# Optimization experiments

Measured on AMD Instinct MI355X. Metric: run time of the kernel, lower is better.

The kernel has to match this reference:

```python
import jax, jax.numpy as jnp
import numpy as np

B, S, HID = 1, 2048, 2048
N_HEADS = 16
HEAD_DIM = HID // N_HEADS  # 128
ROPE_THETA = 10000.0
NEG_INF = -1e9


def setup_inputs() -> dict:
    key = jax.random.key(0)
    ks = jax.random.split(key, 5)
    hidden_states = jax.random.normal(ks[0], (B, S, HID), dtype=jnp.float32)
    scale = 1.0 / np.sqrt(HID)
    Wq = jax.random.normal(ks[1], (HID, HID), dtype=jnp.float32) * scale
    Wk = jax.random.normal(ks[2], (HID, HID), dtype=jnp.float32) * scale
    Wv = jax.random.normal(ks[3], (HID, HID), dtype=jnp.float32) * scale
    Wo = jax.random.normal(ks[4], (HID, HID), dtype=jnp.float32) * scale
    # additive causal mask [B, 1, S, S]: 0 on/below diag, -1e9 above
    causal = jnp.tril(jnp.ones((S, S), dtype=bool))
    attention_mask = jnp.where(causal, 0.0, NEG_INF).astype(jnp.float32)[None, None]
    attention_mask = jnp.broadcast_to(attention_mask, (B, 1, S, S))
    position_ids = jnp.broadcast_to(jnp.arange(S, dtype=jnp.int64)[None, :], (B, S))
    return {"hidden_states": hidden_states, "Wq": Wq, "Wk": Wk, "Wv": Wv,
            "Wo": Wo, "attention_mask": attention_mask, "position_ids": position_ids}


def _rotate_half(x):
    x1, x2 = jnp.split(x, 2, axis=-1)
    return jnp.concatenate((-x2, x1), axis=-1)


def _rope_cos_sin(position_ids, head_dim, dtype):
    inv_freq = 1.0 / (ROPE_THETA ** (jnp.arange(0, head_dim, 2, dtype=jnp.float32) / head_dim))
    freqs = position_ids.astype(jnp.float32)[:, :, None] * inv_freq[None, None, :]  # [b, s, d/2]
    emb = jnp.concatenate((freqs, freqs), axis=-1)  # [b, s, d]
    # unsqueeze_dim=1 -> broadcast over heads
    return jnp.cos(emb).astype(dtype)[:, None], jnp.sin(emb).astype(dtype)[:, None]


def reference(hidden_states, Wq, Wk, Wv, Wo, attention_mask, position_ids):
    b, s, h = hidden_states.shape
    d = HEAD_DIM
    def proj(W):
        return (hidden_states @ W.T).reshape(b, s, N_HEADS, d).transpose(0, 2, 1, 3)  # [b,h,s,d]
    q, k, v = proj(Wq), proj(Wk), proj(Wv)
    cos, sin = _rope_cos_sin(position_ids, d, q.dtype)
    q = q * cos + _rotate_half(q) * sin
    k = k * cos + _rotate_half(k) * sin
    scores = jnp.einsum('bhqd,bhkd->bhqk', q, k) / jnp.sqrt(jnp.float32(d))
    scores = scores + attention_mask
    probs = jax.nn.softmax(scores.astype(jnp.float32), axis=-1).astype(q.dtype)
    attn = jnp.einsum('bhqk,bhkd->bhqd', probs, v)
    out = attn.transpose(0, 2, 1, 3).reshape(b, s, h)
    return out @ Wo.T
```

## Files before the change

### kernel.cpp

```cpp
#include <hip/hip_runtime.h>

typedef _Float16 half8 __attribute__((ext_vector_type(8)));
typedef _Float16 half4 __attribute__((ext_vector_type(4)));
typedef float floatx4 __attribute__((ext_vector_type(4)));
typedef float floatx16 __attribute__((ext_vector_type(16)));

#define GLDS(gp, lp) __builtin_amdgcn_global_load_lds( \
    (const __attribute__((address_space(1))) void*)(gp), \
    (__attribute__((address_space(3))) void*)(lp), 16, 0, 0)

__global__ void cvt_f2h5(const float* __restrict__ s0, const float* __restrict__ s1,
                         const float* __restrict__ s2, const float* __restrict__ s3,
                         const float* __restrict__ s4,
                         _Float16* __restrict__ d0, _Float16* __restrict__ d1,
                         _Float16* __restrict__ d2, _Float16* __restrict__ d3,
                         _Float16* __restrict__ d4, int n8) {
  int i = blockIdx.x * 256 + threadIdx.x;
  if (i >= n8) return;
  const float* s; _Float16* d;
  switch (blockIdx.y) {
    case 0: s = s0; d = d0; break;
    case 1: s = s1; d = d1; break;
    case 2: s = s2; d = d2; break;
    case 3: s = s3; d = d3; break;
    default: s = s4; d = d4; break;
  }
  const float4* s4p = (const float4*)s;
  float4 a = s4p[2 * i], b = s4p[2 * i + 1];
  half8 h;
  h[0] = (_Float16)a.x; h[1] = (_Float16)a.y; h[2] = (_Float16)a.z; h[3] = (_Float16)a.w;
  h[4] = (_Float16)b.x; h[5] = (_Float16)b.y; h[6] = (_Float16)b.z; h[7] = (_Float16)b.w;
  *(half8*)(d + 8 * (size_t)i) = h;
}

__global__ __launch_bounds__(256) void rope_tr(_Float16* __restrict__ Q,
                                               _Float16* __restrict__ K,
                                               const _Float16* __restrict__ V,
                                               _Float16* __restrict__ Vt) {
  __shared__ _Float16 t[64][72];
  const int bid = (int)blockIdx.x;
  if (bid < 8192) {
    const int idx = bid * 256 + threadIdx.x;
    const int s = idx >> 10;
    const int hd = idx & 1023;
    const int head = hd >> 6, d = hd & 63;
    const float freq = exp2f((float)d * -0.2076205059304601f);
    const float ang = (float)s * freq;
    float sn, c;
    __sincosf(ang, &sn, &c);
    const size_t base = (size_t)s * 2048 + head * 128 + d;
    float q1 = (float)Q[base], q2 = (float)Q[base + 64];
    Q[base]      = (_Float16)(q1 * c - q2 * sn);
    Q[base + 64] = (_Float16)(q2 * c + q1 * sn);
    float k1 = (float)K[base], k2 = (float)K[base + 64];
    K[base]      = (_Float16)(k1 * c - k2 * sn);
    K[base + 64] = (_Float16)(k2 * c + k1 * sn);
  } else {
    const int b2 = bid - 8192;
    const int r0 = (b2 >> 5) * 64, c0 = (b2 & 31) * 64;
    const int tr = threadIdx.x >> 3, tc = (threadIdx.x & 7) * 8;
    #pragma unroll
    for (int p = 0; p < 2; ++p) {
      half8 v = *(const half8*)(V + (size_t)(r0 + p * 32 + tr) * 2048 + c0 + tc);
      *(half8*)&t[p * 32 + tr][tc] = v;
    }
    __syncthreads();
    #pragma unroll
    for (int p = 0; p < 2; ++p) {
      half8 v;
      #pragma unroll
      for (int j = 0; j < 8; ++j) v[j] = t[tc + j][p * 32 + tr];
      *(half8*)(Vt + (size_t)(c0 + p * 32 + tr) * 2048 + r0 + tc) = v;
    }
  }
}

__global__ __launch_bounds__(512, 1) void gemm_qkv(const _Float16* __restrict__ A,
                                                   const _Float16* __restrict__ W,
                                                   _Float16* __restrict__ Cq) {
  extern __shared__ _Float16 lds[];
  _Float16* As = lds;
  _Float16* Bs = lds + 3 * 16384;

  const int tid = threadIdx.x, lane = tid & 63, wv = tid >> 6;
  const int fr = lane & 15, fg = lane >> 4;
  const int wm = wv >> 1, wn = wv & 1;
  const int bm = blockIdx.y * 256, bn = blockIdx.x * 192;
  const _Float16* Ab = A + (size_t)bm * 2048;
  const _Float16* Bb = W + (size_t)bn * 2048;

  const int srow = lane >> 3;
  const int sgr = (lane & 7) ^ srow;

  auto stageA = [&](int t) {
    _Float16* dst = As + (t % 3) * 16384;
    const size_t coff = (size_t)t * 64 + sgr * 8;
    #pragma unroll
    for (int i = 0; i < 4; ++i) {
      const int rb = wv * 32 + i * 8;
      GLDS(Ab + (size_t)(rb + srow) * 2048 + coff, dst + rb * 64);
    }
  };
  auto stageB = [&](int t) {
    _Float16* dst = Bs + (t & 1) * 12288;
    const size_t coff = (size_t)t * 64 + sgr * 8;
    #pragma unroll
    for (int i = 0; i < 3; ++i) {
      const int rb = wv * 24 + i * 8;
      GLDS(Bb + (size_t)(rb + srow) * 2048 + coff, dst + rb * 64);
    }
  };

  const int arow = wm * 64 + fr;
  const int brow = wn * 96 + fr;
  const int sw = fr & 7;

  floatx4 acc[4][6] = {};

  stageA(0); stageB(0); stageA(1);
  asm volatile("s_waitcnt vmcnt(4)" ::: "memory");
  __builtin_amdgcn_s_barrier();

  for (int t = 0; t < 32; ++t) {
    const _Float16* Ac = As + (t % 3) * 16384;
    const _Float16* Bc = Bs + (t & 1) * 12288;
    half8 af[2][4], bf[2][6];
    #pragma unroll
    for (int kh = 0; kh < 2; ++kh) {
      const int sl = ((kh * 4 + fg) ^ sw) * 8;
      #pragma unroll
      for (int m = 0; m < 4; ++m)
        af[kh][m] = *(const half8*)(Ac + (arow + m * 16) * 64 + sl);
      #pragma unroll
      for (int n = 0; n < 6; ++n)
        bf[kh][n] = *(const half8*)(Bc + (brow + n * 16) * 64 + sl);
    }
    if (t + 1 < 32) stageB(t + 1);
    if (t + 2 < 32) stageA(t + 2);
    __builtin_amdgcn_s_setprio(1);
    #pragma unroll
    for (int kh = 0; kh < 2; ++kh)
      #pragma unroll
      for (int m = 0; m < 4; ++m)
        #pragma unroll
        for (int n = 0; n < 6; ++n)
          acc[m][n] = __builtin_amdgcn_mfma_f32_16x16x32_f16(af[kh][m], bf[kh][n],
                                                             acc[m][n], 0, 0, 0);
    __builtin_amdgcn_s_setprio(0);
    if (t < 30)       asm volatile("s_waitcnt vmcnt(4)" ::: "memory");
    else if (t == 30) asm volatile("s_waitcnt vmcnt(0)" ::: "memory");
    __builtin_amdgcn_s_barrier();
  }

  #pragma unroll
  for (int m = 0; m < 4; ++m)
    #pragma unroll
    for (int n = 0; n < 6; ++n)
      #pragma unroll
      for (int i = 0; i < 4; ++i) {
        const int row = bm + wm * 64 + m * 16 + fg * 4 + i;
        const int col = bn + wn * 96 + n * 16 + fr;
        Cq[(size_t)(col >> 11) * 4194304 + (size_t)row * 2048 + (col & 2047)] =
            (_Float16)acc[m][n][i];
      }
}

__global__ __launch_bounds__(256, 3) void gemm_o(const _Float16* __restrict__ A,
                                                 const _Float16* __restrict__ B,
                                                 float* __restrict__ out) {
  extern __shared__ _Float16 lds[];
  _Float16* As = lds;
  _Float16* Bs = lds + 3 * 4096;

  const int tid = threadIdx.x, lane = tid & 63, wv = tid >> 6;
  const int fr = lane & 15, fg = lane >> 4;
  const int wm = (wv >> 1) * 64, wn = (wv & 1) * 64;
  const int bm = blockIdx.y * 128, bn = blockIdx.x * 128;
  const _Float16* Ab = A + (size_t)bm * 2048;
  const _Float16* Bb = B + (size_t)bn * 2048;

  const int srow = lane >> 2;
  const int gsw = (lane & 3) ^ ((lane >> 3) & 3);
  const int asw = (fr >> 1) & 3;

  auto stageA = [&](int t) {
    _Float16* dst = As + (t % 3) * 4096;
    const size_t coff = (size_t)t * 32 + gsw * 8;
    #pragma unroll
    for (int i = 0; i < 2; ++i) {
      const int rb = wv * 32 + i * 16;
      GLDS(Ab + (size_t)(rb + srow) * 2048 + coff, dst + rb * 32);
    }
  };
  auto stageB = [&](int t) {
    _Float16* dst = Bs + (t % 3) * 4096;
    const size_t coff = (size_t)t * 32 + gsw * 8;
    #pragma unroll
    for (int i = 0; i < 2; ++i) {
      const int rb = wv * 32 + i * 16;
      GLDS(Bb + (size_t)(rb + srow) * 2048 + coff, dst + rb * 32);
    }
  };

  floatx4 acc[4][4] = {};

  stageA(0); stageB(0); stageA(1); stageB(1);
  asm volatile("s_waitcnt vmcnt(4)" ::: "memory");
  __builtin_amdgcn_s_barrier();

  for (int t = 0; t < 64; ++t) {
    const _Float16* Ac = As + (t % 3) * 4096;
    const _Float16* Bc = Bs + (t % 3) * 4096;
    half8 af[4], bf[4];
    #pragma unroll
    for (int m = 0; m < 4; ++m)
      af[m] = *(const half8*)(Ac + (wm + m * 16 + fr) * 32 + ((fg ^ asw) * 8));
    #pragma unroll
    for (int n = 0; n < 4; ++n)
      bf[n] = *(const half8*)(Bc + (wn + n * 16 + fr) * 32 + ((fg ^ asw) * 8));
    if (t + 2 < 64) { stageA(t + 2); stageB(t + 2); }
    __builtin_amdgcn_s_setprio(1);
    #pragma unroll
    for (int m = 0; m < 4; ++m)
      #pragma unroll
      for (int n = 0; n < 4; ++n)
        acc[m][n] = __builtin_amdgcn_mfma_f32_16x16x32_f16(af[m], bf[n], acc[m][n], 0, 0, 0);
    __builtin_amdgcn_s_setprio(0);
    if (t < 62) asm volatile("s_waitcnt vmcnt(4)" ::: "memory");
    else        asm volatile("s_waitcnt vmcnt(0)" ::: "memory");
    __builtin_amdgcn_s_barrier();
  }

  #pragma unroll
  for (int m = 0; m < 4; ++m)
    #pragma unroll
    for (int n = 0; n < 4; ++n)
      #pragma unroll
      for (int i = 0; i < 4; ++i) {
        const int row = bm + wm + m * 16 + fg * 4 + i;
        const int col = bn + wn + n * 16 + fr;
        out[(size_t)row * 2048 + col] = acc[m][n][i];
      }
}

__global__ __launch_bounds__(256, 2) void attn_k(const _Float16* __restrict__ Qp,
                                                 const _Float16* __restrict__ Kp,
                                                 const _Float16* __restrict__ Vt,
                                                 _Float16* __restrict__ Po,
                                                 float* __restrict__ Pr) {
  extern __shared__ _Float16 smem[];
  _Float16* Ks = smem;
  _Float16* Vs = smem + 2 * 64 * 128;
  _Float16* Pb = smem + 4 * 64 * 128;

  const int tid = threadIdx.x, lane = tid & 63, wv = tid >> 6;
  const int l31 = lane & 31, hi = lane >> 5;
  const int wq = wv >> 1, wk = wv & 1;

  const int bid = (int)blockIdx.x;
  const int head = ((bid & 7) << 1) | ((bid >> 3) & 1);
  const int L = bid >> 4;
  int g, it0, itEnd;
  if (L < 16) { g = 16 + L; it0 = 0; itEnd = 16; }
  else {
    const int j = (L - 16) >> 1;
    if ((L & 1) == 0) { g = 15 - j; it0 = 0; itEnd = g + 1; }
    else             { g = 31 - j; it0 = 16; itEnd = g + 1; }
  }
  const size_t hoff = (size_t)head * 128;
  const int qw = g * 64 + wq * 32;
  _Float16* Pw = Pb + wv * (32 * 40);

  half8 qf[8];
  const _Float16 scl = (_Float16)0.08838834764831845f;
  #pragma unroll
  for (int ks = 0; ks < 8; ++ks) {
    half8 t = *(const half8*)(Qp + (size_t)(qw + l31) * 2048 + hoff + ks * 16 + hi * 8);
    #pragma unroll
    for (int j = 0; j < 8; ++j) t[j] = (_Float16)(t[j] * scl);
    qf[ks] = t;
  }

  auto stage = [&](int buf, int it) {
    const int kv0 = it * 64;
    #pragma unroll
    for (int i = 0; i < 4; ++i) {
      const int rbase = wv * 16 + i * 4;
      const int row = rbase + (lane >> 4);
      const int gr = (lane & 15) ^ (row & 7);
      GLDS(Kp + (size_t)(kv0 + row) * 2048 + hoff + gr * 8,
           Ks + buf * 8192 + rbase * 128);
    }
    #pragma unroll
    for (int i = 0; i < 4; ++i) {
      const int rbase = wv * 32 + i * 8;
      const int row = rbase + (lane >> 3);
      const int gr = (lane & 7) ^ (row & 7);
      GLDS(Vt + (size_t)(hoff + row) * 2048 + kv0 + gr * 8,
           Vs + buf * 8192 + rbase * 64);
    }
  };

  floatx16 o[4] = {};
  float rsum = 0.0f;

  stage(0, it0);
  asm volatile("s_waitcnt vmcnt(0)" ::: "memory");
  __builtin_amdgcn_s_barrier();

  int buf = 0;
  for (int it = it0; it < itEnd; ++it) {
    if (it + 1 < itEnd) stage(buf ^ 1, it + 1);
    const _Float16* Kb = Ks + buf * 8192;
    const _Float16* Vb = Vs + buf * 8192;

    const int krow = wk * 32 + l31;
    const int ksw = l31 & 7;
    floatx16 S = {};
    __builtin_amdgcn_s_setprio(1);
    #pragma unroll
    for (int ks = 0; ks < 8; ++ks) {
      half8 a = *(const half8*)(Kb + krow * 128 + (((ks * 2 + hi) ^ ksw) * 8));
      S = __builtin_amdgcn_mfma_f32_32x32x16_f16(a, qf[ks], S, 0, 0, 0);
    }
    __builtin_amdgcn_s_setprio(0);

    if (it == g) {
      const int kv0 = it * 64;
      const int qa = qw + l31;
      #pragma unroll
      for (int r = 0; r < 16; ++r) {
        const int ka = kv0 + wk * 32 + (r & 3) + 8 * (r >> 2) + 4 * hi;
        if (ka > qa) S[r] = -1e30f;
      }
    }

    #pragma unroll
    for (int r4 = 0; r4 < 4; ++r4) {
      float p0 = __expf(S[4 * r4 + 0] - 8.0f);
      float p1 = __expf(S[4 * r4 + 1] - 8.0f);
      float p2 = __expf(S[4 * r4 + 2] - 8.0f);
      float p3 = __expf(S[4 * r4 + 3] - 8.0f);
      rsum += (p0 + p1) + (p2 + p3);
      half4 pk;
      pk[0] = (_Float16)p0; pk[1] = (_Float16)p1;
      pk[2] = (_Float16)p2; pk[3] = (_Float16)p3;
      *(half4*)(Pw + l31 * 40 + r4 * 8 + hi * 4) = pk;
    }

    half8 pa0 = *(const half8*)(Pw + l31 * 40 + hi * 8);
    half8 pa1 = *(const half8*)(Pw + l31 * 40 + 16 + hi * 8);

    __builtin_amdgcn_s_setprio(1);
    #pragma unroll
    for (int dt = 0; dt < 4; ++dt) {
      const int vrow = dt * 32 + l31;
      const int vsw = vrow & 7;
      half8 b0 = *(const half8*)(Vb + vrow * 64 + (((wk * 4 + hi) ^ vsw) * 8));
      half8 b1 = *(const half8*)(Vb + vrow * 64 + (((wk * 4 + 2 + hi) ^ vsw) * 8));
      o[dt] = __builtin_amdgcn_mfma_f32_32x32x16_f16(pa0, b0, o[dt], 0, 0, 0);
      o[dt] = __builtin_amdgcn_mfma_f32_32x32x16_f16(pa1, b1, o[dt], 0, 0, 0);
    }
    __builtin_amdgcn_s_setprio(0);

    asm volatile("s_waitcnt vmcnt(0)" ::: "memory");
    __builtin_amdgcn_s_barrier();
    buf ^= 1;
  }

  float* Mo = (float*)smem;
  float* Mr = (float*)(smem + 16384);
  if (wk == 1) {
    #pragma unroll
    for (int dt = 0; dt < 4; ++dt)
      #pragma unroll
      for (int r = 0; r < 16; ++r)
        Mo[((wq * 4 + dt) * 16 + r) * 64 + lane] = o[dt][r];
    Mr[wq * 64 + lane] = rsum;
  }
  __syncthreads();
  if (wk == 0) {
    rsum += Mr[wq * 64 + lane];
    float rs = rsum;
    rs += __shfl_xor(rs, 32);
    if (hi == 0) Pr[(size_t)bid * 64 + wq * 32 + l31] = rs;
    #pragma unroll
    for (int dt = 0; dt < 4; ++dt)
      #pragma unroll
      for (int r = 0; r < 16; ++r) {
        const float w = o[dt][r] + Mo[((wq * 4 + dt) * 16 + r) * 64 + lane];
        const int ql = wq * 32 + (r & 3) + 8 * (r >> 2) + 4 * hi;
        Po[(size_t)bid * 8192 + ql * 128 + dt * 32 + l31] = (_Float16)w;
      }
  }
}

__global__ __launch_bounds__(256) void attn_merge(const _Float16* __restrict__ Po,
                                                  const float* __restrict__ Pr,
                                                  _Float16* __restrict__ At) {
  const int bidx = (int)blockIdx.x;
  const int h = bidx & 15, g = bidx >> 4;
  const int hb = ((h & 1) << 3) | (h >> 1);
  const int L0 = (g >= 16) ? (g - 16) : (16 + 2 * (15 - g));
  const int U0 = L0 * 16 + hb;
  const bool two = (g >= 16);
  const int U1 = two ? ((17 + 2 * (31 - g)) * 16 + hb) : 0;
  const int t = threadIdx.x;
  const int q = t >> 2, cs = t & 3;
  const float r0 = Pr[(size_t)U0 * 64 + q];
  const float r1 = two ? Pr[(size_t)U1 * 64 + q] : 0.0f;
  const float inv = 1.0f / (r0 + r1);
  const size_t orow = (size_t)(g * 64 + q) * 2048 + h * 128;
  #pragma unroll
  for (int s = 0; s < 4; ++s) {
    const int d0 = (cs + s * 4) * 8;
    half8 a = *(const half8*)(Po + (size_t)U0 * 8192 + q * 128 + d0);
    half8 o;
    if (two) {
      half8 b = *(const half8*)(Po + (size_t)U1 * 8192 + q * 128 + d0);
      #pragma unroll
      for (int j = 0; j < 8; ++j) o[j] = (_Float16)(((float)a[j] + (float)b[j]) * inv);
    } else {
      #pragma unroll
      for (int j = 0; j < 8; ++j) o[j] = (_Float16)((float)a[j] * inv);
    }
    *(half8*)(At + orow + d0) = o;
  }
}

extern "C" void kernel_launch(void* const* d_in, const int* in_sizes, int n_in,
                              void* d_out, int out_size, void* d_ws, size_t ws_size,
                              hipStream_t stream) {
  (void)in_sizes; (void)n_in; (void)out_size; (void)ws_size;
  const float* X  = (const float*)d_in[0];
  const float* Wq = (const float*)d_in[1];
  const float* Wk = (const float*)d_in[2];
  const float* Wv = (const float*)d_in[3];
  const float* Wo = (const float*)d_in[4];
  float* out = (float*)d_out;

  const size_t SZ = 2048ull * 2048ull;
  _Float16* ws  = (_Float16*)d_ws;
  _Float16* Xh  = ws + 0 * SZ;
  _Float16* Wqh = ws + 1 * SZ;
  _Float16* Wkh = ws + 2 * SZ;
  _Float16* Wvh = ws + 3 * SZ;
  _Float16* Woh = ws + 4 * SZ;
  _Float16* Qp  = ws + 5 * SZ;
  _Float16* Kp  = ws + 6 * SZ;
  _Float16* Vp  = ws + 7 * SZ;
  _Float16* Vtg = Wqh;
  _Float16* At  = Xh;
  _Float16* Po  = Wkh;
  float*    Pr  = (float*)Vp;

  const int n8 = (int)(SZ / 8);
  dim3 blk(256);

  cvt_f2h5<<<dim3(n8 / 256, 5), blk, 0, stream>>>(X, Wq, Wk, Wv, Wo,
                                                  Xh, Wqh, Wkh, Wvh, Woh, n8);

  gemm_qkv<<<dim3(32, 8), dim3(512), 147456, stream>>>(Xh, Wqh, Qp);

  rope_tr<<<8192 + 1024, blk, 0, stream>>>(Qp, Kp, Vp, Vtg);

  const size_t attn_lds = (4 * 64 * 128 + 4 * 32 * 40) * sizeof(_Float16);
  attn_k<<<768, blk, attn_lds, stream>>>(Qp, Kp, Vtg, Po, Pr);
  attn_merge<<<512, blk, 0, stream>>>(Po, Pr, At);

  gemm_o<<<dim3(16, 16), blk, 49152, stream>>>(At, Woh, out);
}
```

Before: 149.0 us.

## Fuse Q RoPE into attention and normalize unsplit rows in-kernel

Q rotary embedding is moved out of the rope kernel and applied in registers while attn_k loads Q, folded together with the softmax scale. This removes a full read-modify-write pass over Q. Blocks that cover a query tile's whole key range now normalize and write straight to the attention output, so attn_merge only runs for the split tiles and launches half the blocks. The cost is extra sincos work per attention block and two output paths in the epilogue.

```diff
diff --git a/kernel.cpp b/kernel.cpp
--- a/kernel.cpp
+++ b/kernel.cpp
@@ -33,8 +33,7 @@
   *(half8*)(d + 8 * (size_t)i) = h;
 }
 
-__global__ __launch_bounds__(256) void rope_tr(_Float16* __restrict__ Q,
-                                               _Float16* __restrict__ K,
+__global__ __launch_bounds__(256) void rope_tr(_Float16* __restrict__ K,
                                                const _Float16* __restrict__ V,
                                                _Float16* __restrict__ Vt) {
   __shared__ _Float16 t[64][72];
@@ -49,9 +48,6 @@
     float sn, c;
     __sincosf(ang, &sn, &c);
     const size_t base = (size_t)s * 2048 + head * 128 + d;
-    float q1 = (float)Q[base], q2 = (float)Q[base + 64];
-    Q[base]      = (_Float16)(q1 * c - q2 * sn);
-    Q[base + 64] = (_Float16)(q2 * c + q1 * sn);
     float k1 = (float)K[base], k2 = (float)K[base + 64];
     K[base]      = (_Float16)(k1 * c - k2 * sn);
     K[base + 64] = (_Float16)(k2 * c + k1 * sn);
@@ -247,7 +243,8 @@
                                                  const _Float16* __restrict__ Kp,
                                                  const _Float16* __restrict__ Vt,
                                                  _Float16* __restrict__ Po,
-                                                 float* __restrict__ Pr) {
+                                                 float* __restrict__ Pr,
+                                                 _Float16* __restrict__ At) {
   extern __shared__ _Float16 smem[];
   _Float16* Ks = smem;
   _Float16* Vs = smem + 2 * 64 * 128;
@@ -267,18 +264,29 @@
     if ((L & 1) == 0) { g = 15 - j; it0 = 0; itEnd = g + 1; }
     else             { g = 31 - j; it0 = 16; itEnd = g + 1; }
   }
+  const bool full = (it0 == 0) && (itEnd == g + 1);
   const size_t hoff = (size_t)head * 128;
   const int qw = g * 64 + wq * 32;
   _Float16* Pw = Pb + wv * (32 * 40);
 
   half8 qf[8];
-  const _Float16 scl = (_Float16)0.08838834764831845f;
   #pragma unroll
-  for (int ks = 0; ks < 8; ++ks) {
-    half8 t = *(const half8*)(Qp + (size_t)(qw + l31) * 2048 + hoff + ks * 16 + hi * 8);
-    #pragma unroll
-    for (int j = 0; j < 8; ++j) t[j] = (_Float16)(t[j] * scl);
-    qf[ks] = t;
+  for (int ks = 0; ks < 8; ++ks)
+    qf[ks] = *(const half8*)(Qp + (size_t)(qw + l31) * 2048 + hoff + ks * 16 + hi * 8);
+  {
+    const float qrow = (float)(qw + l31);
+    #pragma unroll
+    for (int ks = 0; ks < 4; ++ks)
+      #pragma unroll
+      for (int j = 0; j < 8; ++j) {
+        const int d = ks * 16 + hi * 8 + j;
+        const float fq = exp2f((float)d * -0.2076205059304601f);
+        float sn, c;
+        __sincosf(qrow * fq, &sn, &c);
+        const float q0 = (float)qf[ks][j], q1 = (float)qf[ks + 4][j];
+        qf[ks][j]     = (_Float16)((q0 * c - q1 * sn) * 0.08838834764831845f);
+        qf[ks + 4][j] = (_Float16)((q1 * c + q0 * sn) * 0.08838834764831845f);
+      }
   }
 
   auto stage = [&](int buf, int it) {
@@ -383,15 +391,31 @@
     rsum += Mr[wq * 64 + lane];
     float rs = rsum;
     rs += __shfl_xor(rs, 32);
-    if (hi == 0) Pr[(size_t)bid * 64 + wq * 32 + l31] = rs;
-    #pragma unroll
-    for (int dt = 0; dt < 4; ++dt)
-      #pragma unroll
-      for (int r = 0; r < 16; ++r) {
-        const float w = o[dt][r] + Mo[((wq * 4 + dt) * 16 + r) * 64 + lane];
-        const int ql = wq * 32 + (r & 3) + 8 * (r >> 2) + 4 * hi;
-        Po[(size_t)bid * 8192 + ql * 128 + dt * 32 + l31] = (_Float16)w;
-      }
+    if (full) {
+      const float inv = 1.0f / rs;
+      float invq[16];
+      #pragma unroll
+      for (int r = 0; r < 16; ++r)
+        invq[r] = __shfl(inv, (r & 3) + 8 * (r >> 2) + 4 * hi, 32);
+      #pragma unroll
+      for (int dt = 0; dt < 4; ++dt)
+        #pragma unroll
+        for (int r = 0; r < 16; ++r) {
+          const float w = (o[dt][r] + Mo[((wq * 4 + dt) * 16 + r) * 64 + lane]) * invq[r];
+          const int qa = qw + (r & 3) + 8 * (r >> 2) + 4 * hi;
+          At[(size_t)qa * 2048 + hoff + dt * 32 + l31] = (_Float16)w;
+        }
+    } else {
+      if (hi == 0) Pr[(size_t)bid * 64 + wq * 32 + l31] = rs;
+      #pragma unroll
+      for (int dt = 0; dt < 4; ++dt)
+        #pragma unroll
+        for (int r = 0; r < 16; ++r) {
+          const float w = o[dt][r] + Mo[((wq * 4 + dt) * 16 + r) * 64 + lane];
+          const int ql = wq * 32 + (r & 3) + 8 * (r >> 2) + 4 * hi;
+          Po[(size_t)bid * 8192 + ql * 128 + dt * 32 + l31] = (_Float16)w;
+        }
+    }
   }
 }
 
@@ -399,31 +423,24 @@
                                                   const float* __restrict__ Pr,
                                                   _Float16* __restrict__ At) {
   const int bidx = (int)blockIdx.x;
-  const int h = bidx & 15, g = bidx >> 4;
+  const int h = bidx & 15, g = 16 + (bidx >> 4);
   const int hb = ((h & 1) << 3) | (h >> 1);
-  const int L0 = (g >= 16) ? (g - 16) : (16 + 2 * (15 - g));
-  const int U0 = L0 * 16 + hb;
-  const bool two = (g >= 16);
-  const int U1 = two ? ((17 + 2 * (31 - g)) * 16 + hb) : 0;
+  const int U0 = (g - 16) * 16 + hb;
+  const int U1 = (17 + 2 * (31 - g)) * 16 + hb;
   const int t = threadIdx.x;
   const int q = t >> 2, cs = t & 3;
   const float r0 = Pr[(size_t)U0 * 64 + q];
-  const float r1 = two ? Pr[(size_t)U1 * 64 + q] : 0.0f;
+  const float r1 = Pr[(size_t)U1 * 64 + q];
   const float inv = 1.0f / (r0 + r1);
   const size_t orow = (size_t)(g * 64 + q) * 2048 + h * 128;
   #pragma unroll
   for (int s = 0; s < 4; ++s) {
     const int d0 = (cs + s * 4) * 8;
     half8 a = *(const half8*)(Po + (size_t)U0 * 8192 + q * 128 + d0);
+    half8 b = *(const half8*)(Po + (size_t)U1 * 8192 + q * 128 + d0);
     half8 o;
-    if (two) {
-      half8 b = *(const half8*)(Po + (size_t)U1 * 8192 + q * 128 + d0);
-      #pragma unroll
-      for (int j = 0; j < 8; ++j) o[j] = (_Float16)(((float)a[j] + (float)b[j]) * inv);
-    } else {
-      #pragma unroll
-      for (int j = 0; j < 8; ++j) o[j] = (_Float16)((float)a[j] * inv);
-    }
+    #pragma unroll
+    for (int j = 0; j < 8; ++j) o[j] = (_Float16)(((float)a[j] + (float)b[j]) * inv);
     *(half8*)(At + orow + d0) = o;
   }
 }
@@ -462,11 +479,11 @@
 
   gemm_qkv<<<dim3(32, 8), dim3(512), 147456, stream>>>(Xh, Wqh, Qp);
 
-  rope_tr<<<8192 + 1024, blk, 0, stream>>>(Qp, Kp, Vp, Vtg);
+  rope_tr<<<8192 + 1024, blk, 0, stream>>>(Kp, Vp, Vtg);
 
   const size_t attn_lds = (4 * 64 * 128 + 4 * 32 * 40) * sizeof(_Float16);
-  attn_k<<<768, blk, attn_lds, stream>>>(Qp, Kp, Vtg, Po, Pr);
-  attn_merge<<<512, blk, 0, stream>>>(Po, Pr, At);
+  attn_k<<<768, blk, attn_lds, stream>>>(Qp, Kp, Vtg, Po, Pr, At);
+  attn_merge<<<256, blk, 0, stream>>>(Po, Pr, At);
 
   gemm_o<<<dim3(16, 16), blk, 49152, stream>>>(At, Woh, out);
 }
```

Result: no change. 150.3 us, median of 2 (+0.9%).
